# Kernel tuning notes

Hardware: AMD Instinct MI355X
Metric: run time of the kernel (lower is better)

Reference implementation:

```python
import jax, jax.numpy as jnp
import numpy as np

RES = 64

TRI_TABLE = jnp.array([
    [-1,-1,-1,-1,-1,-1],[1,0,2,-1,-1,-1],[4,0,3,-1,-1,-1],[1,4,2,1,3,4],
    [3,1,5,-1,-1,-1],[2,3,0,2,5,3],[1,4,0,1,5,4],[4,2,5,-1,-1,-1],
    [4,5,2,-1,-1,-1],[4,1,0,4,5,1],[3,2,0,3,5,2],[1,3,5,-1,-1,-1],
    [4,1,2,4,3,1],[3,0,4,-1,-1,-1],[2,0,1,-1,-1,-1],[-1,-1,-1,-1,-1,-1]], dtype=jnp.int32)
NUM_TRI = jnp.array([0,1,1,2,1,2,2,1,1,2,2,1,2,1,1,0], dtype=jnp.int32)
BASE_EDGES = jnp.array([0,1,0,2,0,3,1,2,1,3,2,3], dtype=jnp.int32)


def _make_tet_grid(res):
    # Kuhn 6-tet decomposition of each cube of a (res+1)^3 grid.
    n = res + 1
    ii, jj, kk = np.meshgrid(np.arange(n), np.arange(n), np.arange(n), indexing='ij')
    verts = (np.stack([ii, jj, kk], -1).reshape(-1, 3).astype(np.float32)) / res
    def vid(i, j, k):
        return (i * n + j) * n + k
    i, j, k = np.meshgrid(np.arange(res), np.arange(res), np.arange(res), indexing='ij')
    i, j, k = i.ravel(), j.ravel(), k.ravel()
    c = [vid(i + (b & 1), j + ((b >> 1) & 1), k + ((b >> 2) & 1)) for b in range(8)]
    kuhn = [(0,1,3,7),(0,3,2,7),(0,2,6,7),(0,6,4,7),(0,4,5,7),(0,5,1,7)]
    tets = np.stack([np.stack([c[a], c[b], c[d], c[e]], -1) for (a, b, d, e) in kuhn], 1)
    return verts, tets.reshape(-1, 4).astype(np.int64)


def setup_inputs() -> dict:
    key = jax.random.key(0)
    verts, tets = _make_tet_grid(RES)
    level = jax.random.normal(key, (verts.shape[0], 1), dtype=jnp.float32)
    return {"level": level, "pos": jnp.asarray(verts), "tet": jnp.asarray(tets), "threshold": 0}


def reference(level, pos, tet, threshold):
    sdf = level - threshold                    # [N,1]
    occ = sdf[:, 0] > 0                        # [N]
    occ_fx4 = occ[tet]                         # [F,4]
    occ_sum = occ_fx4.sum(-1)
    valid = (occ_sum > 0) & (occ_sum < 4)
    vt = tet[valid]                            # [Fv,4]
    occ_valid = occ_fx4[valid]                 # [Fv,4]

    edges = jnp.sort(vt[:, BASE_EDGES].reshape(-1, 2), axis=1)   # [Fv*6,2]
    unique_edges, idx_map = jnp.unique(edges, axis=0, return_inverse=True)
    idx_map = idx_map.reshape(-1)
    mask_edges = occ[unique_edges].sum(-1) == 1                  # crossing edges
    mapping = jnp.where(mask_edges, jnp.cumsum(mask_edges) - 1, -1)
    idx_map = mapping[idx_map].reshape(-1, 6)                    # [Fv,6]
    interp_v = unique_edges[mask_edges]                          # [M,2]

    p = pos[interp_v]                                            # [M,2,3]
    s = sdf[interp_v][..., 0] * jnp.array([1.0, -1.0], dtype=sdf.dtype)  # [M,2]
    w = s[:, ::-1] / s.sum(1, keepdims=True)                     # flip / denom
    verts_out = (p * w[..., None]).sum(1)                        # [M,3]

    v_id = 2 ** jnp.arange(4, dtype=jnp.int32)
    tetindex = (occ_valid.astype(jnp.int32) * v_id).sum(-1)      # [Fv]
    num_tri = NUM_TRI[tetindex]
    m1, m2 = num_tri == 1, num_tri == 2
    f1 = jnp.take_along_axis(idx_map[m1], TRI_TABLE[tetindex[m1]][:, :3], axis=1).reshape(-1, 3)
    f2 = jnp.take_along_axis(idx_map[m2], TRI_TABLE[tetindex[m2]][:, :6], axis=1).reshape(-1, 3)
    faces = jnp.concatenate([f1, f2], axis=0)
    return verts_out, faces
```

## Files before the change

kernel.cpp:

```cpp
#include <hip/hip_runtime.h>


#define RESX 64
#define NV   65
#define NV2  4225
#define NVERT 274625
#define NCUBE 262144
#define BLOCK 256
#define NBLK 1073
#define CBLK 1024
#define WINW 20
#define STAGE 9216

__constant__ int c_tri[16][6] = {
    {-1,-1,-1,-1,-1,-1},{1,0,2,-1,-1,-1},{4,0,3,-1,-1,-1},{1,4,2,1,3,4},
    {3,1,5,-1,-1,-1},{2,3,0,2,5,3},{1,4,0,1,5,4},{4,2,5,-1,-1,-1},
    {4,5,2,-1,-1,-1},{4,1,0,4,5,1},{3,2,0,3,5,2},{1,3,5,-1,-1,-1},
    {4,1,2,4,3,1},{3,0,4,-1,-1,-1},{2,0,1,-1,-1,-1},{-1,-1,-1,-1,-1,-1}};
__constant__ int c_ntri[16] = {0,1,1,2,1,2,2,1,1,2,2,1,2,1,1,0};
__constant__ int c_kuhn[6][4] = {{0,1,3,7},{0,3,2,7},{0,2,6,7},{0,6,4,7},{0,4,5,7},{0,5,1,7}};
__constant__ int c_off8[8] = {0,4225,65,4290,1,4226,66,4291};
__constant__ int c_loc[6][6] = {
    {0,0,0,1,1,3},{0,0,0,2,3,2},{0,0,0,2,2,6},
    {0,0,0,4,6,4},{0,0,0,4,4,5},{0,0,0,1,5,1}};
__constant__ int c_dir[6][6] = {
    {3,5,6,1,2,0},{5,1,6,3,0,4},{1,2,6,0,4,3},
    {2,0,6,1,3,5},{0,4,6,3,5,1},{4,3,6,0,1,2}};

__device__ __forceinline__ unsigned block_reduce(unsigned v, unsigned* lds) {
    int tid = threadIdx.x, lane = tid & 63, w = tid >> 6;
#pragma unroll
    for (int off = 32; off > 0; off >>= 1)
        v += (unsigned)__shfl_xor((int)v, off, 64);
    if (lane == 0) lds[w] = v;
    __syncthreads();
    if (tid == 0) lds[4] = lds[0] + lds[1] + lds[2] + lds[3];
    __syncthreads();
    return lds[4];
}

__device__ __forceinline__ unsigned block_scan_excl(unsigned val, unsigned* lds,
                                                    unsigned& block_total) {
    int tid = threadIdx.x, lane = tid & 63, w = tid >> 6;
    unsigned x = val;
#pragma unroll
    for (int off = 1; off < 64; off <<= 1) {
        unsigned y = (unsigned)__shfl_up((int)x, off, 64);
        if (lane >= off) x += y;
    }
    if (lane == 63) lds[w] = x;
    __syncthreads();
    if (tid == 0) {
        unsigned s = 0;
#pragma unroll
        for (int i = 0; i < 4; i++) { unsigned t = lds[i]; lds[i + 4] = s; s += t; }
        lds[8] = s;
    }
    __syncthreads();
    block_total = lds[8];
    return x - val + lds[4 + w];
}

__global__ void __launch_bounds__(256)
pass1(const float* __restrict__ level, const float* __restrict__ thrp,
      unsigned char* __restrict__ flagsArr, unsigned short* __restrict__ locEx,
      unsigned* __restrict__ bsE, unsigned* __restrict__ bsT) {
    __shared__ unsigned lds[9];
    __shared__ unsigned ldsc[5];
    int tid = threadIdx.x;
    int bid = blockIdx.x;
    int gid = bid * BLOCK + tid;
    float thr = thrp[0];

    unsigned fl = 0;
    if (gid < NVERT) {
        int i = gid / NV2; int r = gid - i * NV2; int j = r / NV; int k = r - j * NV;
        bool okx = i < RESX, oky = j < RESX, okz = k < RESX;
        float v0 = level[gid] - thr;
        bool s0 = v0 > 0.f;
        fl = s0 ? 0x80u : 0u;
        const int b2d[8] = {0, 3, 1, 5, 0, 4, 2, 6};
#pragma unroll
        for (int b = 1; b < 8; b++) {
            bool ok = (!(b & 1) || okx) && (!(b & 2) || oky) && (!(b & 4) || okz);
            if (ok) {
                float vb = level[gid + c_off8[b]] - thr;
                if ((vb > 0.f) != s0) fl |= (1u << b2d[b]);
            }
        }
        flagsArr[gid] = (unsigned char)fl;
    }
    unsigned cnt = __popc(fl & 0x7fu);
    unsigned totE;
    unsigned ex = block_scan_excl(cnt, lds, totE);
    if (gid < NVERT) locEx[gid] = (unsigned short)ex;
    if (tid == 0) bsE[bid] = totE;

    unsigned tv = 0;
    if (gid < NCUBE) {
        int ci = gid >> 12, cj = (gid >> 6) & 63, ck = gid & 63;
        int base = (ci * NV + cj) * NV + ck;
        unsigned occ8 = 0;
#pragma unroll
        for (int b = 0; b < 8; b++)
            occ8 |= ((level[base + c_off8[b]] - thr) > 0.f ? 1u : 0u) << b;
        unsigned c1 = 0, c2 = 0;
#pragma unroll
        for (int t = 0; t < 6; t++) {
            int cfg = ((occ8 >> c_kuhn[t][0]) & 1) | (((occ8 >> c_kuhn[t][1]) & 1) << 1)
                    | (((occ8 >> c_kuhn[t][2]) & 1) << 2) | (((occ8 >> c_kuhn[t][3]) & 1) << 3);
            int nt = c_ntri[cfg];
            c1 += (nt == 1); c2 += (nt == 2);
        }
        tv = c1 | (c2 << 16);
    }
    unsigned totC = block_reduce(tv, ldsc);
    if (tid == 0) bsT[bid] = totC;
}

__global__ void __launch_bounds__(256)
pass2(const float* __restrict__ level, const float* __restrict__ thrp,
      const unsigned char* __restrict__ flagsArr,
      const unsigned short* __restrict__ locEx,
      const unsigned* __restrict__ bsE, const unsigned* __restrict__ bsT,
      float* __restrict__ out) {
    __shared__ unsigned lds[9];
    __shared__ unsigned ldsc[5];
    __shared__ unsigned win[WINW];
    __shared__ unsigned pEw[WINW];
    __shared__ float stage[STAGE];
    int tid = threadIdx.x;
    int bid = blockIdx.x;
    int gid = bid * BLOCK + tid;
    float thr = thrp[0];

    int g0 = bid << 8;
    int wci = g0 >> 12, wcj = (g0 >> 6) & 63;
    int wb = (bid < CBLK) ? (((wci * NV + wcj) * NV) >> 8) : 0;

    unsigned lE = 0, lEp = 0, lWb = 0, l1 = 0, l1p = 0, l2p = 0;
    for (int t = tid; t < NBLK; t += BLOCK) {
        unsigned e = bsE[t], c = bsT[t];
        lE += e; l1 += c & 0xffffu;
        if (t < bid) { lEp += e; l1p += c & 0xffffu; l2p += c >> 16; }
        if (t < wb)  { lWb += e; }
    }
    if (tid < WINW) {
        int t = wb + tid;
        win[tid] = (t < NBLK) ? bsE[t] : 0u;
    }
    unsigned M    = block_reduce(lE,  ldsc);
    unsigned pE   = block_reduce(lEp, ldsc);
    unsigned C1   = block_reduce(l1,  ldsc);
    unsigned p1b  = block_reduce(l1p, ldsc);
    unsigned p2b  = block_reduce(l2p, ldsc);
    unsigned wAcc = block_reduce(lWb, ldsc);
    if (tid < WINW) {
        unsigned s = wAcc;
        for (int d = 0; d < tid; d++) s += win[d];
        pEw[tid] = s;
    }

    unsigned totE = bsE[bid];
    if (gid < NVERT) {
        unsigned fl = flagsArr[gid];
        if (fl & 0x7fu) {
            int i = gid / NV2; int r = gid - i * NV2; int j = r / NV; int k = r - j * NV;
            float v0 = level[gid] - thr;
            unsigned slot = locEx[gid];
            const float inv = 1.f / 64.f;
            const int d2b[7] = {4, 2, 6, 1, 5, 3, 7};
            float fi = (float)i, fj = (float)j, fk = (float)k;
#pragma unroll
            for (int d = 0; d < 7; d++) {
                if (fl & (1u << d)) {
                    const int b = d2b[d];
                    float s1 = level[gid + c_off8[b]] - thr;
                    float denom = v0 - s1;
                    float w0 = (-s1) / denom;
                    float w1 = v0 / denom;
                    float* o = &stage[3u * slot];
                    o[0] = (fi * w0 + (fi + (float)(b & 1)) * w1) * inv;
                    o[1] = (fj * w0 + (fj + (float)((b >> 1) & 1)) * w1) * inv;
                    o[2] = (fk * w0 + (fk + (float)((b >> 2) & 1)) * w1) * inv;
                    slot++;
                }
            }
        }
    }
    __syncthreads();
    {
        float* dst = out + 3u * pE;
        unsigned n = totE * 3u;
        for (unsigned idx = tid; idx < n; idx += BLOCK)
            __builtin_nontemporal_store(stage[idx], &dst[idx]);
    }

    if (bid >= CBLK) return;
    __syncthreads();

    int ci = gid >> 12, cj = (gid >> 6) & 63, ck = gid & 63;
    int base = (ci * NV + cj) * NV + ck;
    unsigned long long f8 = 0ull;
#pragma unroll
    for (int b = 0; b < 8; b++)
        f8 |= (unsigned long long)flagsArr[base + c_off8[b]] << (8 * b);
    unsigned occ8 = 0;
#pragma unroll
    for (int b = 0; b < 8; b++) occ8 |= (unsigned)((f8 >> (8 * b + 7)) & 1ull) << b;
    int cfgs[6], nts[6];
    unsigned c1 = 0, c2 = 0;
#pragma unroll
    for (int t = 0; t < 6; t++) {
        int cfg = ((occ8 >> c_kuhn[t][0]) & 1) | (((occ8 >> c_kuhn[t][1]) & 1) << 1)
                | (((occ8 >> c_kuhn[t][2]) & 1) << 2) | (((occ8 >> c_kuhn[t][3]) & 1) << 3);
        cfgs[t] = cfg;
        int nt = c_ntri[cfg];
        nts[t] = nt;
        c1 += (nt == 1); c2 += (nt == 2);
    }
    unsigned tot2;
    unsigned ex2 = block_scan_excl(c1 | (c2 << 16), lds, tot2);
    unsigned f1 = tot2 & 0xffffu;
    unsigned f2 = tot2 >> 16;
    unsigned l1c = ex2 & 0xffffu;
    unsigned l2c = ex2 >> 16;
    unsigned n1 = f1 * 3u;
#pragma unroll
    for (int t = 0; t < 6; t++) {
        int nt = nts[t];
        if (nt == 0) continue;
        int cfg = cfgs[t];
        unsigned basef = (nt == 1) ? (3u * l1c) : (n1 + 6u * l2c);
        int cntm = 3 * nt;
        for (int m = 0; m < cntm; m++) {
            int e = c_tri[cfg][m];
            int lc = c_loc[t][e];
            int dir = c_dir[t][e];
            int lo = base + c_off8[lc];
            unsigned flb = (unsigned)((f8 >> (8 * lc)) & 0xffull);
            unsigned rnk = pEw[(lo >> 8) - wb] + locEx[lo]
                         + __popc(flb & ((1u << dir) - 1u));
            stage[basef + (unsigned)m] = (float)rnk;
        }
        l1c += (nt == 1);
        l2c += (nt == 2);
    }
    __syncthreads();
    float* of = out + 3ull * M;
    float* o1 = of + 3u * p1b;
    for (unsigned idx = tid; idx < n1; idx += BLOCK)
        __builtin_nontemporal_store(stage[idx], &o1[idx]);
    unsigned n2 = f2 * 6u;
    float* o2 = of + 3u * (C1 + 2u * p2b);
    for (unsigned idx = tid; idx < n2; idx += BLOCK)
        __builtin_nontemporal_store(stage[n1 + idx], &o2[idx]);
}

extern "C" void kernel_launch(void* const* d_in, const int* in_sizes, int n_in,
                              void* d_out, int out_size, void* d_ws, size_t ws_size,
                              hipStream_t stream) {
    const float* level = (const float*)d_in[0];
    const float* thrp = (const float*)d_in[3];
    float* out = (float*)d_out;

    char* p = (char*)d_ws;
    unsigned char* flagsArr = (unsigned char*)p;
    p += (NVERT + 255) & ~255;
    unsigned short* locEx = (unsigned short*)p;
    p += ((sizeof(unsigned short) * NVERT) + 255) & ~255;
    unsigned* bsE = (unsigned*)p;  p += sizeof(unsigned) * NBLK;
    unsigned* bsT = (unsigned*)p;

    pass1<<<NBLK, BLOCK, 0, stream>>>(level, thrp, flagsArr, locEx, bsE, bsT);
    pass2<<<NBLK, BLOCK, 0, stream>>>(level, thrp, flagsArr, locEx, bsE, bsT, out);
}
```

Measured before the change: 117.7 us.

## Process four vertices per thread in pass1 with wave-level scans and packed block sums

```diff
diff --git a/kernel.cpp b/kernel.cpp
--- a/kernel.cpp
+++ b/kernel.cpp
@@ -7,10 +7,13 @@
 #define NVERT 274625
 #define NCUBE 262144
 #define BLOCK 256
-#define NBLK 1073
+#define NGRP 1073
+#define CGRP 1024
+#define NBLK1 269
 #define CBLK 1024
 #define WINW 20
 #define STAGE 9216
+#define M21 0x1fffffu
 
 __constant__ int c_tri[16][6] = {
     {-1,-1,-1,-1,-1,-1},{1,0,2,-1,-1,-1},{4,0,3,-1,-1,-1},{1,4,2,1,3,4},
@@ -27,11 +30,14 @@
     {3,5,6,1,2,0},{5,1,6,3,0,4},{1,2,6,0,4,3},
     {2,0,6,1,3,5},{0,4,6,3,5,1},{4,3,6,0,1,2}};
 
-__device__ __forceinline__ unsigned block_reduce(unsigned v, unsigned* lds) {
+typedef unsigned long long u64;
+#define NTRI_PACK 0x16696994u
+
+__device__ __forceinline__ u64 block_reduce_u64(u64 v, u64* lds) {
     int tid = threadIdx.x, lane = tid & 63, w = tid >> 6;
 #pragma unroll
     for (int off = 32; off > 0; off >>= 1)
-        v += (unsigned)__shfl_xor((int)v, off, 64);
+        v += __shfl_xor(v, off, 64);
     if (lane == 0) lds[w] = v;
     __syncthreads();
     if (tid == 0) lds[4] = lds[0] + lds[1] + lds[2] + lds[3];
@@ -64,68 +70,140 @@
 __global__ void __launch_bounds__(256)
 pass1(const float* __restrict__ level, const float* __restrict__ thrp,
       unsigned char* __restrict__ flagsArr, unsigned short* __restrict__ locEx,
-      unsigned* __restrict__ bsE, unsigned* __restrict__ bsT) {
-    __shared__ unsigned lds[9];
-    __shared__ unsigned ldsc[5];
-    int tid = threadIdx.x;
-    int bid = blockIdx.x;
-    int gid = bid * BLOCK + tid;
+      u64* __restrict__ bsAll) {
+    int tid = threadIdx.x, lane = tid & 63, w = tid >> 6;
+    int group = blockIdx.x * 4 + w;
+    if (group >= NGRP) return;
     float thr = thrp[0];
 
-    unsigned fl = 0;
-    if (gid < NVERT) {
-        int i = gid / NV2; int r = gid - i * NV2; int j = r / NV; int k = r - j * NV;
-        bool okx = i < RESX, oky = j < RESX, okz = k < RESX;
-        float v0 = level[gid] - thr;
-        bool s0 = v0 > 0.f;
-        fl = s0 ? 0x80u : 0u;
+    int v = group * 256 + lane * 4;
+    unsigned fl[4] = {0, 0, 0, 0};
+    if (v <= NVERT - 4295) {
+        float r0[5], rY[5], rX[5], rXY[5];
+#pragma unroll
+        for (int e = 0; e < 5; e++) {
+            r0[e]  = level[v + e]        - thr;
+            rY[e]  = level[v + 65 + e]   - thr;
+            rX[e]  = level[v + 4225 + e] - thr;
+            rXY[e] = level[v + 4290 + e] - thr;
+        }
+        int i0 = v / NV2; int r = v - i0 * NV2; int j0 = r / NV; int k0 = r - j0 * NV;
+#pragma unroll
+        for (int d = 0; d < 4; d++) {
+            int kk = k0 + d, jj = j0;
+            if (kk > 64) { kk -= 65; jj += 1; }
+            if (jj > 64) { jj -= 65; }
+            bool oky = jj < RESX, okz = kk < RESX;
+            bool s0 = r0[d] > 0.f;
+            unsigned f = s0 ? 0x80u : 0u;
+            if (okz &&        ((r0[d+1]  > 0.f) != s0)) f |= 1u;
+            if (oky &&        ((rY[d]    > 0.f) != s0)) f |= 2u;
+            if (oky && okz && ((rY[d+1]  > 0.f) != s0)) f |= 4u;
+            if (              ((rX[d]    > 0.f) != s0)) f |= 8u;
+            if (okz &&        ((rX[d+1]  > 0.f) != s0)) f |= 16u;
+            if (oky &&        ((rXY[d]   > 0.f) != s0)) f |= 32u;
+            if (oky && okz && ((rXY[d+1] > 0.f) != s0)) f |= 64u;
+            fl[d] = f;
+        }
+    } else {
         const int b2d[8] = {0, 3, 1, 5, 0, 4, 2, 6};
 #pragma unroll
-        for (int b = 1; b < 8; b++) {
-            bool ok = (!(b & 1) || okx) && (!(b & 2) || oky) && (!(b & 4) || okz);
-            if (ok) {
-                float vb = level[gid + c_off8[b]] - thr;
-                if ((vb > 0.f) != s0) fl |= (1u << b2d[b]);
+        for (int d = 0; d < 4; d++) {
+            int g = v + d;
+            if (g >= NVERT) continue;
+            int i = g / NV2; int r = g - i * NV2; int j = r / NV; int k = r - j * NV;
+            bool okx = i < RESX, oky = j < RESX, okz = k < RESX;
+            float s = level[g] - thr;
+            bool s0 = s > 0.f;
+            unsigned f = s0 ? 0x80u : 0u;
+#pragma unroll
+            for (int b = 1; b < 8; b++) {
+                bool ok = (!(b & 1) || okx) && (!(b & 2) || oky) && (!(b & 4) || okz);
+                if (ok) {
+                    float vb = level[g + c_off8[b]] - thr;
+                    if ((vb > 0.f) != s0) f |= (1u << b2d[b]);
+                }
             }
-        }
-        flagsArr[gid] = (unsigned char)fl;
-    }
-    unsigned cnt = __popc(fl & 0x7fu);
-    unsigned totE;
-    unsigned ex = block_scan_excl(cnt, lds, totE);
-    if (gid < NVERT) locEx[gid] = (unsigned short)ex;
-    if (tid == 0) bsE[bid] = totE;
-
-    unsigned tv = 0;
-    if (gid < NCUBE) {
-        int ci = gid >> 12, cj = (gid >> 6) & 63, ck = gid & 63;
+            fl[d] = f;
+        }
+    }
+    unsigned cnt[4];
+#pragma unroll
+    for (int d = 0; d < 4; d++) cnt[d] = __popc(fl[d] & 0x7fu);
+    unsigned cth = cnt[0] + cnt[1] + cnt[2] + cnt[3];
+    unsigned x = cth;
+#pragma unroll
+    for (int off = 1; off < 64; off <<= 1) {
+        unsigned y = (unsigned)__shfl_up((int)x, off, 64);
+        if (lane >= off) x += y;
+    }
+    unsigned wex = x - cth;
+    unsigned totE = (unsigned)__shfl((int)x, 63, 64);
+    if (v + 3 < NVERT) {
+        *(uchar4*)(flagsArr + v) = make_uchar4((unsigned char)fl[0], (unsigned char)fl[1],
+                                               (unsigned char)fl[2], (unsigned char)fl[3]);
+        ushort4 e4;
+        e4.x = (unsigned short)wex;
+        e4.y = (unsigned short)(wex + cnt[0]);
+        e4.z = (unsigned short)(wex + cnt[0] + cnt[1]);
+        e4.w = (unsigned short)(wex + cnt[0] + cnt[1] + cnt[2]);
+        *(ushort4*)(locEx + v) = e4;
+    } else {
+        unsigned e = wex;
+        for (int d = 0; d < 4; d++) {
+            int g = v + d;
+            if (g < NVERT) {
+                flagsArr[g] = (unsigned char)fl[d];
+                locEx[g] = (unsigned short)e;
+                e += cnt[d];
+            }
+        }
+    }
+
+    unsigned c1 = 0, c2 = 0;
+    if (group < CGRP) {
+        int c0 = group * 256 + lane * 4;
+        int ci = c0 >> 12, cj = (c0 >> 6) & 63, ck = c0 & 63;
         int base = (ci * NV + cj) * NV + ck;
-        unsigned occ8 = 0;
-#pragma unroll
-        for (int b = 0; b < 8; b++)
-            occ8 |= ((level[base + c_off8[b]] - thr) > 0.f ? 1u : 0u) << b;
-        unsigned c1 = 0, c2 = 0;
-#pragma unroll
-        for (int t = 0; t < 6; t++) {
-            int cfg = ((occ8 >> c_kuhn[t][0]) & 1) | (((occ8 >> c_kuhn[t][1]) & 1) << 1)
-                    | (((occ8 >> c_kuhn[t][2]) & 1) << 2) | (((occ8 >> c_kuhn[t][3]) & 1) << 3);
-            int nt = c_ntri[cfg];
-            c1 += (nt == 1); c2 += (nt == 2);
-        }
-        tv = c1 | (c2 << 16);
-    }
-    unsigned totC = block_reduce(tv, ldsc);
-    if (tid == 0) bsT[bid] = totC;
+        float q0[5], qY[5], qX[5], qXY[5];
+#pragma unroll
+        for (int e = 0; e < 5; e++) {
+            q0[e]  = level[base + e]        - thr;
+            qY[e]  = level[base + 65 + e]   - thr;
+            qX[e]  = level[base + 4225 + e] - thr;
+            qXY[e] = level[base + 4290 + e] - thr;
+        }
+#pragma unroll
+        for (int d = 0; d < 4; d++) {
+            unsigned occ8 = (q0[d]   > 0.f ?   1u : 0u) | (qX[d]   > 0.f ?   2u : 0u)
+                          | (qY[d]   > 0.f ?   4u : 0u) | (qXY[d]  > 0.f ?   8u : 0u)
+                          | (q0[d+1] > 0.f ?  16u : 0u) | (qX[d+1] > 0.f ?  32u : 0u)
+                          | (qY[d+1] > 0.f ?  64u : 0u) | (qXY[d+1]> 0.f ? 128u : 0u);
+#pragma unroll
+            for (int t = 0; t < 6; t++) {
+                int cfg = ((occ8 >> c_kuhn[t][0]) & 1) | (((occ8 >> c_kuhn[t][1]) & 1) << 1)
+                        | (((occ8 >> c_kuhn[t][2]) & 1) << 2) | (((occ8 >> c_kuhn[t][3]) & 1) << 3);
+                unsigned nt = (NTRI_PACK >> (cfg << 1)) & 3u;
+                c1 += (nt == 1);
+                c2 += (nt == 2);
+            }
+        }
+        unsigned pk = c1 | (c2 << 16);
+#pragma unroll
+        for (int off = 32; off; off >>= 1) pk += (unsigned)__shfl_xor((int)pk, off, 64);
+        c1 = pk & 0xffffu; c2 = pk >> 16;
+    }
+    if (lane == 0)
+        bsAll[group] = (u64)totE | ((u64)c1 << 16) | ((u64)c2 << 32);
 }
 
 __global__ void __launch_bounds__(256)
 pass2(const float* __restrict__ level, const float* __restrict__ thrp,
       const unsigned char* __restrict__ flagsArr,
       const unsigned short* __restrict__ locEx,
-      const unsigned* __restrict__ bsE, const unsigned* __restrict__ bsT,
-      float* __restrict__ out) {
+      const u64* __restrict__ bsAll, float* __restrict__ out) {
     __shared__ unsigned lds[9];
-    __shared__ unsigned ldsc[5];
+    __shared__ u64 lds64[5];
     __shared__ unsigned win[WINW];
     __shared__ unsigned pEw[WINW];
     __shared__ float stage[STAGE];
@@ -139,29 +217,34 @@
     int wb = (bid < CBLK) ? (((wci * NV + wcj) * NV) >> 8) : 0;
 
     unsigned lE = 0, lEp = 0, lWb = 0, l1 = 0, l1p = 0, l2p = 0;
-    for (int t = tid; t < NBLK; t += BLOCK) {
-        unsigned e = bsE[t], c = bsT[t];
-        lE += e; l1 += c & 0xffffu;
-        if (t < bid) { lEp += e; l1p += c & 0xffffu; l2p += c >> 16; }
+    for (int t = tid; t < NGRP; t += BLOCK) {
+        u64 a = bsAll[t];
+        unsigned e  = (unsigned)a & 0xffffu;
+        unsigned x1 = (unsigned)(a >> 16) & 0xffffu;
+        unsigned x2 = (unsigned)(a >> 32) & 0xffffu;
+        lE += e; l1 += x1;
+        if (t < bid) { lEp += e; l1p += x1; l2p += x2; }
         if (t < wb)  { lWb += e; }
     }
     if (tid < WINW) {
         int t = wb + tid;
-        win[tid] = (t < NBLK) ? bsE[t] : 0u;
-    }
-    unsigned M    = block_reduce(lE,  ldsc);
-    unsigned pE   = block_reduce(lEp, ldsc);
-    unsigned C1   = block_reduce(l1,  ldsc);
-    unsigned p1b  = block_reduce(l1p, ldsc);
-    unsigned p2b  = block_reduce(l2p, ldsc);
-    unsigned wAcc = block_reduce(lWb, ldsc);
+        win[tid] = (t < NGRP) ? ((unsigned)bsAll[t] & 0xffffu) : 0u;
+    }
+    u64 r0 = block_reduce_u64((u64)lE | ((u64)lEp << 21) | ((u64)lWb << 42), lds64);
+    u64 r1 = block_reduce_u64((u64)l1 | ((u64)l1p << 21) | ((u64)l2p << 42), lds64);
+    unsigned M    = (unsigned)r0 & M21;
+    unsigned pE   = (unsigned)(r0 >> 21) & M21;
+    unsigned wAcc = (unsigned)(r0 >> 42);
+    unsigned C1   = (unsigned)r1 & M21;
+    unsigned p1b  = (unsigned)(r1 >> 21) & M21;
+    unsigned p2b  = (unsigned)(r1 >> 42);
     if (tid < WINW) {
         unsigned s = wAcc;
         for (int d = 0; d < tid; d++) s += win[d];
         pEw[tid] = s;
     }
 
-    unsigned totE = bsE[bid];
+    unsigned totE = (unsigned)bsAll[bid] & 0xffffu;
     if (gid < NVERT) {
         unsigned fl = flagsArr[gid];
         if (fl & 0x7fu) {
@@ -176,13 +259,11 @@
                 if (fl & (1u << d)) {
                     const int b = d2b[d];
                     float s1 = level[gid + c_off8[b]] - thr;
-                    float denom = v0 - s1;
-                    float w0 = (-s1) / denom;
-                    float w1 = v0 / denom;
+                    float w1 = v0 * __builtin_amdgcn_rcpf(v0 - s1);
                     float* o = &stage[3u * slot];
-                    o[0] = (fi * w0 + (fi + (float)(b & 1)) * w1) * inv;
-                    o[1] = (fj * w0 + (fj + (float)((b >> 1) & 1)) * w1) * inv;
-                    o[2] = (fk * w0 + (fk + (float)((b >> 2) & 1)) * w1) * inv;
+                    o[0] = (fi + (float)(b & 1) * w1) * inv;
+                    o[1] = (fj + (float)((b >> 1) & 1) * w1) * inv;
+                    o[2] = (fk + (float)((b >> 2) & 1) * w1) * inv;
                     slot++;
                 }
             }
@@ -201,10 +282,10 @@
 
     int ci = gid >> 12, cj = (gid >> 6) & 63, ck = gid & 63;
     int base = (ci * NV + cj) * NV + ck;
-    unsigned long long f8 = 0ull;
+    u64 f8 = 0ull;
 #pragma unroll
     for (int b = 0; b < 8; b++)
-        f8 |= (unsigned long long)flagsArr[base + c_off8[b]] << (8 * b);
+        f8 |= (u64)flagsArr[base + c_off8[b]] << (8 * b);
     unsigned occ8 = 0;
 #pragma unroll
     for (int b = 0; b < 8; b++) occ8 |= (unsigned)((f8 >> (8 * b + 7)) & 1ull) << b;
@@ -269,9 +350,8 @@
     p += (NVERT + 255) & ~255;
     unsigned short* locEx = (unsigned short*)p;
     p += ((sizeof(unsigned short) * NVERT) + 255) & ~255;
-    unsigned* bsE = (unsigned*)p;  p += sizeof(unsigned) * NBLK;
-    unsigned* bsT = (unsigned*)p;
-
-    pass1<<<NBLK, BLOCK, 0, stream>>>(level, thrp, flagsArr, locEx, bsE, bsT);
-    pass2<<<NBLK, BLOCK, 0, stream>>>(level, thrp, flagsArr, locEx, bsE, bsT, out);
-}
+    u64* bsAll = (u64*)p;
+
+    pass1<<<NBLK1, BLOCK, 0, stream>>>(level, thrp, flagsArr, locEx, bsAll);
+    pass2<<<NGRP, BLOCK, 0, stream>>>(level, thrp, flagsArr, locEx, bsAll, out);
+}
```

New measurement: 116.4 us. No clear change (-1.1%).
